# Kernel tuning notes

Hardware: AMD Instinct MI355X
Metric: run time of the kernel (lower is better)

## Reference

```python
import jax, jax.numpy as jnp
import numpy as np

DIM, N_HEADS, N_KV, HEAD_DIM = 5120, 40, 8, 128
MAX_BS, MAX_SEQ = 8, 4096
BSZ, SEQLEN, START_POS = 8, 1, 4095


def setup_inputs() -> dict:
    key = jax.random.key(0)
    ks = jax.random.split(key, 12)
    x = jax.random.normal(ks[0], (BSZ, SEQLEN, DIM), jnp.float32)
    # RoPE angles for positions [START_POS, START_POS+SEQLEN)
    inv_freq = 1.0 / (10000.0 ** (np.arange(0, HEAD_DIM, 2, dtype=np.float32) / HEAD_DIM))
    t = np.arange(START_POS, START_POS + SEQLEN, dtype=np.float32)
    ang = np.outer(t, inv_freq)  # [seqlen, head_dim//2]
    freqs_cis = jnp.asarray(np.stack([np.cos(ang), np.sin(ang)], axis=-1), jnp.float32)
    cache_k = jax.random.normal(ks[1], (MAX_BS, MAX_SEQ, N_KV, HEAD_DIM), jnp.float32)
    cache_v = jax.random.normal(ks[2], (MAX_BS, MAX_SEQ, N_KV, HEAD_DIM), jnp.float32)
    s = 0.02
    wq = jax.random.normal(ks[3], (DIM, N_HEADS * HEAD_DIM), jnp.float32) * s
    bq = jax.random.normal(ks[4], (N_HEADS * HEAD_DIM,), jnp.float32) * s
    wk = jax.random.normal(ks[5], (DIM, N_KV * HEAD_DIM), jnp.float32) * s
    bk = jax.random.normal(ks[6], (N_KV * HEAD_DIM,), jnp.float32) * s
    wv = jax.random.normal(ks[7], (DIM, N_KV * HEAD_DIM), jnp.float32) * s
    bv = jax.random.normal(ks[8], (N_KV * HEAD_DIM,), jnp.float32) * s
    wo = jax.random.normal(ks[9], (N_HEADS * HEAD_DIM, DIM), jnp.float32) * s
    bo = jax.random.normal(ks[10], (DIM,), jnp.float32) * s
    return dict(x=x, start_pos=START_POS, freqs_cis=freqs_cis, cache_k=cache_k,
                cache_v=cache_v, wq=wq, bq=bq, wk=wk, bk=bk, wv=wv, bv=bv, wo=wo, bo=bo)


def _apply_rope(xq, xk, freqs_cis):
    # x*: [b, s, h, hd]; freqs_cis: [s, hd//2, 2] (cos, sin)
    cos = freqs_cis[None, :, None, :, 0]
    sin = freqs_cis[None, :, None, :, 1]
    def rot(x):
        xr = x.reshape(*x.shape[:-1], HEAD_DIM // 2, 2)
        xe, xo = xr[..., 0], xr[..., 1]
        out = jnp.stack([xe * cos - xo * sin, xe * sin + xo * cos], axis=-1)
        return out.reshape(x.shape)
    return rot(xq), rot(xk)


def reference(x, start_pos, freqs_cis, cache_k, cache_v, wq, bq, wk, bk, wv, bv, wo, bo):
    bsz, seqlen, _ = x.shape
    n_rep = N_HEADS // N_KV
    xq = (x @ wq + bq).reshape(bsz, seqlen, N_HEADS, HEAD_DIM)
    xk = (x @ wk + bk).reshape(bsz, seqlen, N_KV, HEAD_DIM)
    xv = (x @ wv + bv).reshape(bsz, seqlen, N_KV, HEAD_DIM)
    xq, xk = _apply_rope(xq, xk, freqs_cis)
    # KV-cache scatter (in-place write in the original)
    cache_k = jax.lax.dynamic_update_slice(cache_k, xk, (0, start_pos, 0, 0))
    cache_v = jax.lax.dynamic_update_slice(cache_v, xv, (0, start_pos, 0, 0))
    klen = start_pos + seqlen
    keys = cache_k[:bsz, :klen]    # [b, t, n_kv, hd]
    values = cache_v[:bsz, :klen]
    # GQA attention without materializing the repeat_kv expansion (same math)
    qg = xq.reshape(bsz, seqlen, N_KV, n_rep, HEAD_DIM)
    scale = 1.0 / np.sqrt(HEAD_DIM)
    scores = jnp.einsum('bsgrd,btgd->bgrst', qg, keys) * scale  # [b,g,r,s,t]
    probs = jax.nn.softmax(scores.astype(jnp.float32), axis=-1).astype(x.dtype)
    out = jnp.einsum('bgrst,btgd->bsgrd', probs, values)
    out = out.reshape(bsz, seqlen, N_HEADS * HEAD_DIM)
    return out @ wo + bo
```

## Files before the change

### kernel.cpp

```cpp
#include <hip/hip_runtime.h>
#include <hip/hip_bf16.h>
#include <math.h>

#define DIM   5120
#define NH    40
#define NKV   8
#define HD    128
#define BS    8
#define KLEN  4096
#define NEWT  4095
#define NREP  5

#define ODQKV 7168
#define NKC   32
#define KCH   (DIM / NKC)

#define NCHUNK 32
#define CH_T   (KLEN / NCHUNK)
#define WAVE_T (CH_T / 4)
#define NPART  NCHUNK

#define WS_Q       0
#define WS_K       (WS_Q + BS * DIM)
#define WS_V       (WS_K + BS * NKV * HD)
#define WS_ATTN    (WS_V + BS * NKV * HD)
#define WS_SCRATCH (WS_ATTN + BS * DIM)

__global__ __launch_bounds__(256) void qkv_partial_k(
    const float* __restrict__ x, const float* __restrict__ wq,
    const float* __restrict__ wk, const float* __restrict__ wv,
    float* __restrict__ part) {
  const int cb = blockIdx.x % 14;
  const int kc = blockIdx.x / 14;
  const int c0 = cb * 512 + threadIdx.x * 2;

  const float* w; int OD, j;
  if (c0 < 5120)      { w = wq; OD = 5120; j = c0; }
  else if (c0 < 6144) { w = wk; OD = 1024; j = c0 - 5120; }
  else                { w = wv; OD = 1024; j = c0 - 6144; }

  const int i0 = kc * KCH;
  float ax[BS], ay[BS];
#pragma unroll
  for (int b = 0; b < BS; ++b) { ax[b] = 0.f; ay[b] = 0.f; }

  const float* wp = w + (size_t)i0 * OD + j;
  const float* xp = x + i0;
#pragma unroll 4
  for (int ii = 0; ii < KCH; ++ii) {
    const float2 wv2 = *(const float2*)&wp[(size_t)ii * OD];
#pragma unroll
    for (int b = 0; b < BS; ++b) {
      const float xb = xp[b * DIM + ii];
      ax[b] = fmaf(xb, wv2.x, ax[b]);
      ay[b] = fmaf(xb, wv2.y, ay[b]);
    }
  }
#pragma unroll
  for (int b = 0; b < BS; ++b)
    *(float2*)&part[((size_t)kc * BS + b) * ODQKV + c0] = make_float2(ax[b], ay[b]);
}

__global__ __launch_bounds__(256) void qkv_reduce_k(
    const float* __restrict__ part, const float* __restrict__ bq,
    const float* __restrict__ bk, const float* __restrict__ bv,
    const float* __restrict__ fc, float* __restrict__ qws,
    float* __restrict__ kws, float* __restrict__ vws) {
  int g = blockIdx.x * 256 + threadIdx.x;
  if (g >= BS * (ODQKV / 2)) return;
  int b  = g / (ODQKV / 2);
  int cp = g - b * (ODQKV / 2);
  int c0 = cp * 2;

  float sx = 0.f, sy = 0.f;
  for (int kc = 0; kc < NKC; ++kc) {
    const float2 p = *(const float2*)&part[((size_t)kc * BS + b) * ODQKV + c0];
    sx += p.x; sy += p.y;
  }

  const float scale = 0.088388347648318447f;
  if (c0 < 5120) {
    sx += bq[c0]; sy += bq[c0 + 1];
    int jf = (c0 & 127) >> 1;
    float cs = fc[2 * jf], sn = fc[2 * jf + 1];
    qws[b * DIM + c0]     = (sx * cs - sy * sn) * scale;
    qws[b * DIM + c0 + 1] = (sx * sn + sy * cs) * scale;
  } else if (c0 < 6144) {
    int jj = c0 - 5120;
    sx += bk[jj]; sy += bk[jj + 1];
    int jf = (jj & 127) >> 1;
    float cs = fc[2 * jf], sn = fc[2 * jf + 1];
    kws[b * NKV * HD + jj]     = sx * cs - sy * sn;
    kws[b * NKV * HD + jj + 1] = sx * sn + sy * cs;
  } else {
    int jj = c0 - 6144;
    vws[b * NKV * HD + jj]     = sx + bv[jj];
    vws[b * NKV * HD + jj + 1] = sy + bv[jj + 1];
  }
}

__global__ __launch_bounds__(256) void attn_partial_k(
    const float* __restrict__ ck, const float* __restrict__ cv,
    const float* __restrict__ qws, const float* __restrict__ kws,
    const float* __restrict__ vws, float* __restrict__ pM,
    float* __restrict__ pL, float* __restrict__ pO) {
  const int blk   = blockIdx.x;
  const int chunk = blk & (NCHUNK - 1);
  const int bh    = blk / NCHUNK;
  const int h     = bh & (NKV - 1);
  const int b     = bh / NKV;
  const int tid   = threadIdx.x;
  const int wave  = tid >> 6;
  const int lane  = tid & 63;
  const int grp   = lane >> 4;
  const int sl    = lane & 15;
  const int t0    = chunk * CH_T + wave * WAVE_T;

  __shared__ float s_lds[CH_T * NREP];
  __shared__ float red[NREP * 8];
  __shared__ float Msh[NREP], Lsh[NREP];
  __shared__ float smO[4][NREP][HD];

  float4 qa[NREP], qb[NREP];
#pragma unroll
  for (int r = 0; r < NREP; ++r) {
    const float* qp = &qws[b * DIM + (h * NREP + r) * HD + 8 * sl];
    qa[r] = *(const float4*)qp;
    qb[r] = *(const float4*)(qp + 4);
  }

  const float* kbase = &ck[((size_t)b * KLEN * NKV + h) * HD];
  const float* vbase = &cv[((size_t)b * KLEN * NKV + h) * HD];

  int niter = WAVE_T / 4;
  const bool tailw = (t0 + WAVE_T == KLEN);
  if (tailw) --niter;

  {
    const float* kp = kbase + (size_t)(t0 + grp) * (NKV * HD) + 8 * sl;
#pragma unroll 4
    for (int i = 0; i < niter; ++i) {
      const float4 ka = *(const float4*)kp;
      const float4 kb = *(const float4*)(kp + 4);
      kp += 4 * NKV * HD;
      float s[NREP];
#pragma unroll
      for (int r = 0; r < NREP; ++r) {
        s[r] = qa[r].x * ka.x + qa[r].y * ka.y + qa[r].z * ka.z + qa[r].w * ka.w
             + qb[r].x * kb.x + qb[r].y * kb.y + qb[r].z * kb.z + qb[r].w * kb.w;
      }
#pragma unroll
      for (int off = 1; off < 16; off <<= 1) {
#pragma unroll
        for (int r = 0; r < NREP; ++r) s[r] += __shfl_xor(s[r], off, 64);
      }
      const int tl = wave * WAVE_T + 4 * i + grp;
      float sv = (sl == 0) ? s[0] : (sl == 1) ? s[1] : (sl == 2) ? s[2]
               : (sl == 3) ? s[3] : s[4];
      if (sl < NREP) s_lds[tl * NREP + sl] = sv;
    }
    if (tailw) {
      const int t  = t0 + WAVE_T - 4 + grp;
      const float* kr = (t == NEWT) ? &kws[(b * NKV + h) * HD]
                                    : kbase + (size_t)t * (NKV * HD);
      const float4 ka = *(const float4*)(kr + 8 * sl);
      const float4 kb = *(const float4*)(kr + 8 * sl + 4);
      float s[NREP];
#pragma unroll
      for (int r = 0; r < NREP; ++r) {
        s[r] = qa[r].x * ka.x + qa[r].y * ka.y + qa[r].z * ka.z + qa[r].w * ka.w
             + qb[r].x * kb.x + qb[r].y * kb.y + qb[r].z * kb.z + qb[r].w * kb.w;
      }
#pragma unroll
      for (int off = 1; off < 16; off <<= 1) {
#pragma unroll
        for (int r = 0; r < NREP; ++r) s[r] += __shfl_xor(s[r], off, 64);
      }
      const int tl = wave * WAVE_T + WAVE_T - 4 + grp;
      float sv = (sl == 0) ? s[0] : (sl == 1) ? s[1] : (sl == 2) ? s[2]
               : (sl == 3) ? s[3] : s[4];
      if (sl < NREP) s_lds[tl * NREP + sl] = sv;
    }
  }
  __syncthreads();

  if (tid < NREP * 8) {
    const int r = tid >> 3, seg = tid & 7;
    float mx = -1e30f;
    for (int k = 0; k < 16; ++k) mx = fmaxf(mx, s_lds[(seg * 16 + k) * NREP + r]);
    red[tid] = mx;
  }
  __syncthreads();
  if (tid < NREP) {
    float mx = red[tid * 8];
    for (int k = 1; k < 8; ++k) mx = fmaxf(mx, red[tid * 8 + k]);
    Msh[tid] = mx;
  }
  __syncthreads();
  for (int idx = tid; idx < CH_T * NREP; idx += 256)
    s_lds[idx] = __expf(s_lds[idx] - Msh[idx % NREP]);
  __syncthreads();
  if (tid < NREP * 8) {
    const int r = tid >> 3, seg = tid & 7;
    float sm = 0.f;
    for (int k = 0; k < 16; ++k) sm += s_lds[(seg * 16 + k) * NREP + r];
    red[tid] = sm;
  }
  __syncthreads();
  if (tid < NREP) {
    float L = 0.f;
    for (int k = 0; k < 8; ++k) L += red[tid * 8 + k];
    Lsh[tid] = L;
  }

  float o[NREP][8];
#pragma unroll
  for (int r = 0; r < NREP; ++r)
#pragma unroll
    for (int j = 0; j < 8; ++j) o[r][j] = 0.f;

  {
    const float* vp = vbase + (size_t)(t0 + grp) * (NKV * HD) + 8 * sl;
#pragma unroll 4
    for (int i = 0; i < niter; ++i) {
      const float4 va = *(const float4*)vp;
      const float4 vb = *(const float4*)(vp + 4);
      vp += 4 * NKV * HD;
      const int tl = wave * WAVE_T + 4 * i + grp;
      float p[NREP];
#pragma unroll
      for (int r = 0; r < NREP; ++r) p[r] = s_lds[tl * NREP + r];
      const float vv[8] = {va.x, va.y, va.z, va.w, vb.x, vb.y, vb.z, vb.w};
#pragma unroll
      for (int r = 0; r < NREP; ++r)
#pragma unroll
        for (int j = 0; j < 8; ++j) o[r][j] = fmaf(p[r], vv[j], o[r][j]);
    }
    if (tailw) {
      const int t  = t0 + WAVE_T - 4 + grp;
      const float* vr = (t == NEWT) ? &vws[(b * NKV + h) * HD]
                                    : vbase + (size_t)t * (NKV * HD);
      const float4 va = *(const float4*)(vr + 8 * sl);
      const float4 vb = *(const float4*)(vr + 8 * sl + 4);
      const int tl = wave * WAVE_T + WAVE_T - 4 + grp;
      float p[NREP];
#pragma unroll
      for (int r = 0; r < NREP; ++r) p[r] = s_lds[tl * NREP + r];
      const float vv[8] = {va.x, va.y, va.z, va.w, vb.x, vb.y, vb.z, vb.w};
#pragma unroll
      for (int r = 0; r < NREP; ++r)
#pragma unroll
        for (int j = 0; j < 8; ++j) o[r][j] = fmaf(p[r], vv[j], o[r][j]);
    }
  }

#pragma unroll
  for (int off = 16; off <= 32; off <<= 1) {
#pragma unroll
    for (int r = 0; r < NREP; ++r)
#pragma unroll
      for (int j = 0; j < 8; ++j) o[r][j] += __shfl_xor(o[r][j], off, 64);
  }

  if (grp == 0) {
#pragma unroll
    for (int r = 0; r < NREP; ++r) {
      float* sp = &smO[wave][r][8 * sl];
      *(float4*)sp       = make_float4(o[r][0], o[r][1], o[r][2], o[r][3]);
      *(float4*)(sp + 4) = make_float4(o[r][4], o[r][5], o[r][6], o[r][7]);
    }
  }
  __syncthreads();

  if (tid < HD) {
    const int d  = tid;
    const int pb = bh * NCHUNK + chunk;
#pragma unroll
    for (int r = 0; r < NREP; ++r) {
      float acc = smO[0][r][d] + smO[1][r][d] + smO[2][r][d] + smO[3][r][d];
      pO[((size_t)pb * NREP + r) * HD + d] = acc;
      if (d == 0) { pM[pb * NREP + r] = Msh[r]; pL[pb * NREP + r] = Lsh[r]; }
    }
  }
}

__global__ __launch_bounds__(256) void attn_combine_k(
    const float* __restrict__ pM, const float* __restrict__ pL,
    const float* __restrict__ pO, float* __restrict__ attn) {
  const int bh  = blockIdx.x;
  const int h   = bh & (NKV - 1);
  const int b   = bh / NKV;
  const int tid = threadIdx.x;
  __shared__ float ml[NREP * NPART], ll[NREP * NPART];
  __shared__ float wgt[NREP * NPART];
  __shared__ float Linv[NREP];

  for (int idx = tid; idx < NREP * NPART; idx += 256) {
    int r = idx / NPART, w = idx - r * NPART;
    ml[idx] = pM[(bh * NPART + w) * NREP + r];
    ll[idx] = pL[(bh * NPART + w) * NREP + r];
  }
  __syncthreads();
  for (int idx = tid; idx < NREP * NPART; idx += 256) {
    int r = idx / NPART;
    float M = -1e30f;
    for (int w = 0; w < NPART; ++w) M = fmaxf(M, ml[r * NPART + w]);
    float e = __expf(ml[idx] - M);
    wgt[idx] = e;
    ll[idx] *= e;
  }
  __syncthreads();
  if (tid < NREP) {
    float L = 0.f;
    for (int w = 0; w < NPART; ++w) L += ll[tid * NPART + w];
    Linv[tid] = 1.f / L;
  }
  __syncthreads();

  for (int oidx = tid; oidx < NREP * HD; oidx += 256) {
    int r = oidx >> 7, d = oidx & 127;
    float acc = 0.f;
    for (int w = 0; w < NPART; ++w)
      acc += wgt[r * NPART + w] * pO[((size_t)(bh * NPART + w) * NREP + r) * HD + d];
    attn[b * DIM + (h * NREP + r) * HD + d] = acc * Linv[r];
  }
}

__global__ __launch_bounds__(256) void out_partial_k(
    const float* __restrict__ attn, const float* __restrict__ wo,
    float* __restrict__ part) {
  const int cb = blockIdx.x % 10;
  const int kc = blockIdx.x / 10;
  const int c0 = cb * 512 + threadIdx.x * 2;

  const int i0 = kc * KCH;
  float ax[BS], ay[BS];
#pragma unroll
  for (int b = 0; b < BS; ++b) { ax[b] = 0.f; ay[b] = 0.f; }

  const float* wp = wo + (size_t)i0 * DIM + c0;
  const float* xp = attn + i0;
#pragma unroll 4
  for (int ii = 0; ii < KCH; ++ii) {
    const float2 wv2 = *(const float2*)&wp[(size_t)ii * DIM];
#pragma unroll
    for (int b = 0; b < BS; ++b) {
      const float xb = xp[b * DIM + ii];
      ax[b] = fmaf(xb, wv2.x, ax[b]);
      ay[b] = fmaf(xb, wv2.y, ay[b]);
    }
  }
#pragma unroll
  for (int b = 0; b < BS; ++b)
    *(float2*)&part[((size_t)kc * BS + b) * DIM + c0] = make_float2(ax[b], ay[b]);
}

__global__ __launch_bounds__(256) void out_reduce_k(
    const float* __restrict__ part, const float* __restrict__ bo,
    float* __restrict__ out) {
  int g = blockIdx.x * 256 + threadIdx.x;
  if (g >= BS * DIM) return;
  int b = g / DIM, c = g - b * DIM;
  float s = 0.f;
  for (int kc = 0; kc < NKC; ++kc) s += part[((size_t)kc * BS + b) * DIM + c];
  out[g] = s + bo[c];
}

extern "C" void kernel_launch(void* const* d_in, const int* in_sizes, int n_in,
                              void* d_out, int out_size, void* d_ws, size_t ws_size,
                              hipStream_t stream) {
  const float* x  = (const float*)d_in[0];
  const float* fc = (const float*)d_in[2];
  const float* ck = (const float*)d_in[3];
  const float* cv = (const float*)d_in[4];
  const float* wq = (const float*)d_in[5];
  const float* bq = (const float*)d_in[6];
  const float* wk = (const float*)d_in[7];
  const float* bk = (const float*)d_in[8];
  const float* wv = (const float*)d_in[9];
  const float* bv = (const float*)d_in[10];
  const float* wo = (const float*)d_in[11];
  const float* bo = (const float*)d_in[12];

  float* ws      = (float*)d_ws;
  float* qws     = ws + WS_Q;
  float* kws     = ws + WS_K;
  float* vws     = ws + WS_V;
  float* attn    = ws + WS_ATTN;
  float* scratch = ws + WS_SCRATCH;

  qkv_partial_k<<<14 * NKC, 256, 0, stream>>>(x, wq, wk, wv, scratch);
  qkv_reduce_k<<<(BS * (ODQKV / 2) + 255) / 256, 256, 0, stream>>>(
      scratch, bq, bk, bv, fc, qws, kws, vws);

  float* pM = scratch;
  float* pL = pM + 64 * NPART * NREP;
  float* pO = pL + 64 * NPART * NREP;
  attn_partial_k<<<64 * NCHUNK, 256, 0, stream>>>(ck, cv, qws, kws, vws, pM, pL, pO);
  attn_combine_k<<<64, 256, 0, stream>>>(pM, pL, pO, attn);

  out_partial_k<<<10 * NKC, 256, 0, stream>>>(attn, wo, scratch);
  out_reduce_k<<<(BS * DIM + 255) / 256, 256, 0, stream>>>(scratch, bo, (float*)d_out);
}
```

Baseline: 130.9 us.

## Stage K chunk into LDS via direct global-to-LDS loads and double chunk count

```diff
diff --git a/kernel.cpp b/kernel.cpp
--- a/kernel.cpp
+++ b/kernel.cpp
@@ -15,16 +15,22 @@
 #define NKC   32
 #define KCH   (DIM / NKC)
 
-#define NCHUNK 32
-#define CH_T   (KLEN / NCHUNK)
-#define WAVE_T (CH_T / 4)
-#define NPART  NCHUNK
+#define NCHB  64
+#define CH_T  (KLEN / NCHB)
+#define NPART NCHB
 
 #define WS_Q       0
 #define WS_K       (WS_Q + BS * DIM)
 #define WS_V       (WS_K + BS * NKV * HD)
 #define WS_ATTN    (WS_V + BS * NKV * HD)
 #define WS_SCRATCH (WS_ATTN + BS * DIM)
+
+__device__ __forceinline__ void gload_lds16(const float* g, float* l) {
+  __builtin_amdgcn_global_load_lds(
+      (const __attribute__((address_space(1))) void*)(unsigned long long)g,
+      (__attribute__((address_space(3))) void*)(unsigned int)(unsigned long long)l,
+      16, 0, 0);
+}
 
 __global__ __launch_bounds__(256) void qkv_partial_k(
     const float* __restrict__ x, const float* __restrict__ wq,
@@ -105,94 +111,82 @@
     const float* __restrict__ vws, float* __restrict__ pM,
     float* __restrict__ pL, float* __restrict__ pO) {
   const int blk   = blockIdx.x;
-  const int chunk = blk & (NCHUNK - 1);
-  const int bh    = blk / NCHUNK;
+  const int chunk = blk & (NCHB - 1);
+  const int bh    = blk / NCHB;
   const int h     = bh & (NKV - 1);
   const int b     = bh / NKV;
   const int tid   = threadIdx.x;
-  const int wave  = tid >> 6;
+  const int w     = tid >> 6;
   const int lane  = tid & 63;
-  const int grp   = lane >> 4;
+  const int g     = lane >> 4;
   const int sl    = lane & 15;
-  const int t0    = chunk * CH_T + wave * WAVE_T;
-
+  const int t0    = chunk * CH_T;
+
+  __shared__ float K_lds[CH_T * HD];
   __shared__ float s_lds[CH_T * NREP];
   __shared__ float red[NREP * 8];
   __shared__ float Msh[NREP], Lsh[NREP];
-  __shared__ float smO[4][NREP][HD];
+
+  {
+    const int hv  = lane >> 5;
+    const int l32 = lane & 31;
+#pragma unroll
+    for (int ii = 0; ii < 8; ++ii) {
+      const int i  = w * 8 + ii;
+      const int r  = 2 * i + hv;
+      const int tg = t0 + r;
+      const float* rowb = (tg == NEWT)
+          ? (kws + (b * NKV + h) * HD)
+          : (ck + (((size_t)b * KLEN + tg) * NKV + h) * HD);
+      const float* src = rowb + 4 * ((l32 - (r & 3)) & 31);
+      gload_lds16(src, &K_lds[i * 256]);
+    }
+  }
 
   float4 qa[NREP], qb[NREP];
 #pragma unroll
-  for (int r = 0; r < NREP; ++r) {
-    const float* qp = &qws[b * DIM + (h * NREP + r) * HD + 8 * sl];
-    qa[r] = *(const float4*)qp;
-    qb[r] = *(const float4*)(qp + 4);
-  }
-
-  const float* kbase = &ck[((size_t)b * KLEN * NKV + h) * HD];
-  const float* vbase = &cv[((size_t)b * KLEN * NKV + h) * HD];
-
-  int niter = WAVE_T / 4;
-  const bool tailw = (t0 + WAVE_T == KLEN);
-  if (tailw) --niter;
-
-  {
-    const float* kp = kbase + (size_t)(t0 + grp) * (NKV * HD) + 8 * sl;
-#pragma unroll 4
-    for (int i = 0; i < niter; ++i) {
-      const float4 ka = *(const float4*)kp;
-      const float4 kb = *(const float4*)(kp + 4);
-      kp += 4 * NKV * HD;
-      float s[NREP];
-#pragma unroll
-      for (int r = 0; r < NREP; ++r) {
-        s[r] = qa[r].x * ka.x + qa[r].y * ka.y + qa[r].z * ka.z + qa[r].w * ka.w
-             + qb[r].x * kb.x + qb[r].y * kb.y + qb[r].z * kb.z + qb[r].w * kb.w;
-      }
-#pragma unroll
-      for (int off = 1; off < 16; off <<= 1) {
-#pragma unroll
-        for (int r = 0; r < NREP; ++r) s[r] += __shfl_xor(s[r], off, 64);
-      }
-      const int tl = wave * WAVE_T + 4 * i + grp;
-      float sv = (sl == 0) ? s[0] : (sl == 1) ? s[1] : (sl == 2) ? s[2]
-               : (sl == 3) ? s[3] : s[4];
-      if (sl < NREP) s_lds[tl * NREP + sl] = sv;
-    }
-    if (tailw) {
-      const int t  = t0 + WAVE_T - 4 + grp;
-      const float* kr = (t == NEWT) ? &kws[(b * NKV + h) * HD]
-                                    : kbase + (size_t)t * (NKV * HD);
-      const float4 ka = *(const float4*)(kr + 8 * sl);
-      const float4 kb = *(const float4*)(kr + 8 * sl + 4);
-      float s[NREP];
-#pragma unroll
-      for (int r = 0; r < NREP; ++r) {
-        s[r] = qa[r].x * ka.x + qa[r].y * ka.y + qa[r].z * ka.z + qa[r].w * ka.w
-             + qb[r].x * kb.x + qb[r].y * kb.y + qb[r].z * kb.z + qb[r].w * kb.w;
-      }
-#pragma unroll
-      for (int off = 1; off < 16; off <<= 1) {
-#pragma unroll
-        for (int r = 0; r < NREP; ++r) s[r] += __shfl_xor(s[r], off, 64);
-      }
-      const int tl = wave * WAVE_T + WAVE_T - 4 + grp;
-      float sv = (sl == 0) ? s[0] : (sl == 1) ? s[1] : (sl == 2) ? s[2]
-               : (sl == 3) ? s[3] : s[4];
-      if (sl < NREP) s_lds[tl * NREP + sl] = sv;
-    }
+  for (int rr = 0; rr < NREP; ++rr) {
+    const float* qp = &qws[b * DIM + (h * NREP + rr) * HD + 8 * sl];
+    qa[rr] = *(const float4*)qp;
+    qb[rr] = *(const float4*)(qp + 4);
+  }
+
+  __syncthreads();
+
+#pragma unroll
+  for (int j = 0; j < 4; ++j) {
+    const int r  = w * 16 + j * 4 + g;
+    const int x0 = (sl * 8 + 4 * g) & 127;
+    const float4 k0 = *(const float4*)&K_lds[r * HD + x0];
+    const float4 k1 = *(const float4*)&K_lds[r * HD + ((x0 + 4) & 127)];
+    float s[NREP];
+#pragma unroll
+    for (int rr = 0; rr < NREP; ++rr) {
+      s[rr] = qa[rr].x * k0.x + qa[rr].y * k0.y + qa[rr].z * k0.z + qa[rr].w * k0.w
+            + qb[rr].x * k1.x + qb[rr].y * k1.y + qb[rr].z * k1.z + qb[rr].w * k1.w;
+    }
+#pragma unroll
+    for (int off = 1; off < 16; off <<= 1) {
+#pragma unroll
+      for (int rr = 0; rr < NREP; ++rr) s[rr] += __shfl_xor(s[rr], off, 64);
+    }
+    float sv = (sl == 0) ? s[0] : (sl == 1) ? s[1] : (sl == 2) ? s[2]
+             : (sl == 3) ? s[3] : s[4];
+    if (sl < NREP) s_lds[r * NREP + sl] = sv;
   }
   __syncthreads();
 
   if (tid < NREP * 8) {
-    const int r = tid >> 3, seg = tid & 7;
+    const int rr = tid >> 3, seg = tid & 7;
     float mx = -1e30f;
-    for (int k = 0; k < 16; ++k) mx = fmaxf(mx, s_lds[(seg * 16 + k) * NREP + r]);
+#pragma unroll
+    for (int k = 0; k < 8; ++k) mx = fmaxf(mx, s_lds[(seg * 8 + k) * NREP + rr]);
     red[tid] = mx;
   }
   __syncthreads();
   if (tid < NREP) {
     float mx = red[tid * 8];
+#pragma unroll
     for (int k = 1; k < 8; ++k) mx = fmaxf(mx, red[tid * 8 + k]);
     Msh[tid] = mx;
   }
@@ -201,85 +195,91 @@
     s_lds[idx] = __expf(s_lds[idx] - Msh[idx % NREP]);
   __syncthreads();
   if (tid < NREP * 8) {
-    const int r = tid >> 3, seg = tid & 7;
+    const int rr = tid >> 3, seg = tid & 7;
     float sm = 0.f;
-    for (int k = 0; k < 16; ++k) sm += s_lds[(seg * 16 + k) * NREP + r];
+#pragma unroll
+    for (int k = 0; k < 8; ++k) sm += s_lds[(seg * 8 + k) * NREP + rr];
     red[tid] = sm;
   }
   __syncthreads();
   if (tid < NREP) {
     float L = 0.f;
+#pragma unroll
     for (int k = 0; k < 8; ++k) L += red[tid * 8 + k];
     Lsh[tid] = L;
   }
 
   float o[NREP][8];
 #pragma unroll
-  for (int r = 0; r < NREP; ++r)
-#pragma unroll
-    for (int j = 0; j < 8; ++j) o[r][j] = 0.f;
-
+  for (int rr = 0; rr < NREP; ++rr)
+#pragma unroll
+    for (int j = 0; j < 8; ++j) o[rr][j] = 0.f;
+
+  const bool tailw = (chunk == NCHB - 1) && (w == 3);
+  const int  jmax  = tailw ? 3 : 4;
   {
-    const float* vp = vbase + (size_t)(t0 + grp) * (NKV * HD) + 8 * sl;
-#pragma unroll 4
-    for (int i = 0; i < niter; ++i) {
+    const float* vp = cv + (((size_t)b * KLEN + (t0 + w * 16 + g)) * NKV + h) * HD + 8 * sl;
+#pragma unroll
+    for (int j = 0; j < jmax; ++j) {
       const float4 va = *(const float4*)vp;
       const float4 vb = *(const float4*)(vp + 4);
-      vp += 4 * NKV * HD;
-      const int tl = wave * WAVE_T + 4 * i + grp;
+      const int r = w * 16 + j * 4 + g;
       float p[NREP];
 #pragma unroll
-      for (int r = 0; r < NREP; ++r) p[r] = s_lds[tl * NREP + r];
+      for (int rr = 0; rr < NREP; ++rr) p[rr] = s_lds[r * NREP + rr];
       const float vv[8] = {va.x, va.y, va.z, va.w, vb.x, vb.y, vb.z, vb.w};
 #pragma unroll
-      for (int r = 0; r < NREP; ++r)
-#pragma unroll
-        for (int j = 0; j < 8; ++j) o[r][j] = fmaf(p[r], vv[j], o[r][j]);
+      for (int rr = 0; rr < NREP; ++rr)
+#pragma unroll
+        for (int jj = 0; jj < 8; ++jj) o[rr][jj] = fmaf(p[rr], vv[jj], o[rr][jj]);
+      vp += (size_t)4 * NKV * HD;
     }
     if (tailw) {
-      const int t  = t0 + WAVE_T - 4 + grp;
-      const float* vr = (t == NEWT) ? &vws[(b * NKV + h) * HD]
-                                    : vbase + (size_t)t * (NKV * HD);
+      const int r  = 60 + g;
+      const int tg = t0 + r;
+      const float* vr = (tg == NEWT) ? (vws + (b * NKV + h) * HD)
+                                     : (cv + (((size_t)b * KLEN + tg) * NKV + h) * HD);
       const float4 va = *(const float4*)(vr + 8 * sl);
       const float4 vb = *(const float4*)(vr + 8 * sl + 4);
-      const int tl = wave * WAVE_T + WAVE_T - 4 + grp;
       float p[NREP];
 #pragma unroll
-      for (int r = 0; r < NREP; ++r) p[r] = s_lds[tl * NREP + r];
+      for (int rr = 0; rr < NREP; ++rr) p[rr] = s_lds[r * NREP + rr];
       const float vv[8] = {va.x, va.y, va.z, va.w, vb.x, vb.y, vb.z, vb.w};
 #pragma unroll
-      for (int r = 0; r < NREP; ++r)
-#pragma unroll
-        for (int j = 0; j < 8; ++j) o[r][j] = fmaf(p[r], vv[j], o[r][j]);
+      for (int rr = 0; rr < NREP; ++rr)
+#pragma unroll
+        for (int jj = 0; jj < 8; ++jj) o[rr][jj] = fmaf(p[rr], vv[jj], o[rr][jj]);
     }
   }
 
 #pragma unroll
   for (int off = 16; off <= 32; off <<= 1) {
 #pragma unroll
-    for (int r = 0; r < NREP; ++r)
-#pragma unroll
-      for (int j = 0; j < 8; ++j) o[r][j] += __shfl_xor(o[r][j], off, 64);
-  }
-
-  if (grp == 0) {
-#pragma unroll
-    for (int r = 0; r < NREP; ++r) {
-      float* sp = &smO[wave][r][8 * sl];
-      *(float4*)sp       = make_float4(o[r][0], o[r][1], o[r][2], o[r][3]);
-      *(float4*)(sp + 4) = make_float4(o[r][4], o[r][5], o[r][6], o[r][7]);
+    for (int rr = 0; rr < NREP; ++rr)
+#pragma unroll
+      for (int jj = 0; jj < 8; ++jj) o[rr][jj] += __shfl_xor(o[rr][jj], off, 64);
+  }
+
+  float* smO = K_lds;
+  if (g == 0) {
+#pragma unroll
+    for (int rr = 0; rr < NREP; ++rr) {
+      float* sp = &smO[(w * NREP + rr) * HD + 8 * sl];
+      *(float4*)sp       = make_float4(o[rr][0], o[rr][1], o[rr][2], o[rr][3]);
+      *(float4*)(sp + 4) = make_float4(o[rr][4], o[rr][5], o[rr][6], o[rr][7]);
     }
   }
   __syncthreads();
 
   if (tid < HD) {
     const int d  = tid;
-    const int pb = bh * NCHUNK + chunk;
-#pragma unroll
-    for (int r = 0; r < NREP; ++r) {
-      float acc = smO[0][r][d] + smO[1][r][d] + smO[2][r][d] + smO[3][r][d];
-      pO[((size_t)pb * NREP + r) * HD + d] = acc;
-      if (d == 0) { pM[pb * NREP + r] = Msh[r]; pL[pb * NREP + r] = Lsh[r]; }
+    const int pb = bh * NCHB + chunk;
+#pragma unroll
+    for (int rr = 0; rr < NREP; ++rr) {
+      float acc = smO[rr * HD + d] + smO[(NREP + rr) * HD + d]
+                + smO[(2 * NREP + rr) * HD + d] + smO[(3 * NREP + rr) * HD + d];
+      pO[((size_t)pb * NREP + rr) * HD + d] = acc;
+      if (d == 0) { pM[pb * NREP + rr] = Msh[rr]; pL[pb * NREP + rr] = Lsh[rr]; }
     }
   }
 }
@@ -396,7 +396,7 @@
   float* pM = scratch;
   float* pL = pM + 64 * NPART * NREP;
   float* pO = pL + 64 * NPART * NREP;
-  attn_partial_k<<<64 * NCHUNK, 256, 0, stream>>>(ck, cv, qws, kws, vws, pM, pL, pO);
+  attn_partial_k<<<64 * NCHB, 256, 0, stream>>>(ck, cv, qws, kws, vws, pM, pL, pO);
   attn_combine_k<<<64, 256, 0, stream>>>(pM, pL, pO, attn);
 
   out_partial_k<<<10 * NKC, 256, 0, stream>>>(attn, wo, scratch);
```

Result: slower. 154.1 us (+17.7%).
